# Performance work log

Hardware: AMD Instinct MI355X
Metric: run time of the kernel (lower is better)

The kernel has to match this reference:

```python
import math
import jax, jax.numpy as jnp
import numpy as np

# ---- static configuration (mirrors init_kwargs / chosen shapes) ----
MUL = 16          # multiplicity in "16x0e+16x1e+16x2e"
B_CFG = 64        # number of configurations in batch
N_ATOM = 64       # atoms per configuration
N_NODES = B_CFG * N_ATOM
N_PAIRS = B_CFG * N_ATOM * N_ATOM

# ---- real Wigner 3j symbols (e3nn convention), computed once in numpy ----
def _su2_cg(j1, m1, j2, m2, j3, m3):
    if m3 != m1 + m2:
        return 0.0
    f = math.factorial
    vmin = max(-j1 + j2 + m3, -j1 + m1, 0)
    vmax = min(j2 + j3 + m1, j3 - j1 + j2, j3 + m3)
    C = math.sqrt((2 * j3 + 1) * f(j3 + j1 - j2) * f(j3 - j1 + j2) * f(j1 + j2 - j3)
                  * f(j3 + m3) * f(j3 - m3)
                  / (f(j1 + j2 + j3 + 1) * f(j1 - m1) * f(j1 + m1) * f(j2 - m2) * f(j2 + m2)))
    S = 0.0
    for v in range(vmin, vmax + 1):
        S += (-1) ** (v + j2 + m2) * f(j2 + j3 + m1 - v) * f(j1 - m1 + v) / (
            f(v) * f(j3 - j1 + j2 - v) * f(j3 + m3 - v) * f(v + j1 - j2 - m3))
    return C * S

def _q_real_to_complex(l):
    q = np.zeros((2 * l + 1, 2 * l + 1), dtype=np.complex128)
    for m in range(-l, 0):
        q[l + m, l + abs(m)] = 1 / 2 ** 0.5
        q[l + m, l - abs(m)] = -1j / 2 ** 0.5
    q[l, l] = 1.0
    for m in range(1, l + 1):
        q[l + m, l + abs(m)] = (-1) ** m / 2 ** 0.5
        q[l + m, l - abs(m)] = 1j * (-1) ** m / 2 ** 0.5
    return (-1j) ** l * q

def _wigner_3j(l1, l2, l3):
    C = np.zeros((2 * l1 + 1, 2 * l2 + 1, 2 * l3 + 1))
    for m1 in range(-l1, l1 + 1):
        for m2 in range(-l2, l2 + 1):
            m3 = m1 + m2
            if abs(m3) <= l3:
                C[l1 + m1, l2 + m2, l3 + m3] = _su2_cg(l1, m1, l2, m2, l3, m3)
    Q1, Q2, Q3 = _q_real_to_complex(l1), _q_real_to_complex(l2), _q_real_to_complex(l3)
    Cr = np.einsum('ij,kl,mn,ikm->jln', Q1, Q2, np.conj(Q3), C.astype(np.complex128))
    assert np.abs(Cr.imag).max() < 1e-6
    Cr = Cr.real
    return Cr / np.linalg.norm(Cr)

# all CG paths (l1, l2, l_out) of the fully connected TP (0e+1e+2e)^2 -> 0e+1e+2e
PATHS = [(0, 0, 0), (1, 1, 0), (2, 2, 0),
         (0, 1, 1), (1, 0, 1), (1, 1, 1), (1, 2, 1), (2, 1, 1), (2, 2, 1),
         (0, 2, 2), (2, 0, 2), (1, 1, 2), (1, 2, 2), (2, 1, 2), (2, 2, 2)]
W3J = {p: _wigner_3j(*p) for p in set(PATHS)}
FAN = {lo: sum(1 for p in PATHS if p[2] == lo) * MUL * MUL for lo in (0, 1, 2)}
ALPHA = {lo: math.sqrt(2 * lo + 1) / math.sqrt(FAN[lo]) for lo in (0, 1, 2)}
# CartesianTensor('ij=ij') change of basis: x_ij = sum_{l,m} QCART[lm,i,j] * irreps[lm]
QCART = np.concatenate([math.sqrt(2 * l + 1) * np.transpose(_wigner_3j(1, 1, l), (2, 0, 1))
                        for l in (0, 1, 2)], axis=0)  # (9, 3, 3), orthonormal rows


def setup_inputs() -> dict:
    key = jax.random.key(0)
    k1, k2 = jax.random.split(key)
    node_feats = jax.random.normal(k1, (N_NODES, MUL * 9), dtype=jnp.float32)
    # layout: for each config, all (i, j) atom pairs with global node indices
    ii, jj = jnp.meshgrid(jnp.arange(N_ATOM, dtype=jnp.int32),
                          jnp.arange(N_ATOM, dtype=jnp.int32), indexing='ij')
    base = (jnp.arange(B_CFG, dtype=jnp.int32) * N_ATOM)[:, None, None]
    rows = (base + ii[None]).reshape(-1)
    cols = (base + jj[None]).reshape(-1)
    layout = jnp.stack([rows, cols], axis=1)  # (N_PAIRS, 2) int32
    tp_weights = jax.random.normal(k2, (len(PATHS), MUL, MUL), dtype=jnp.float32)
    return {'node_feats': node_feats, 'layout': layout, 'tp_weights': tp_weights}


def _split(x):
    # (E, MUL*9) -> {l: (E, MUL, 2l+1)} in irreps order 16x0e | 16x1e | 16x2e
    E = x.shape[0]
    return {0: x[:, :MUL].reshape(E, MUL, 1),
            1: x[:, MUL:4 * MUL].reshape(E, MUL, 3),
            2: x[:, 4 * MUL:].reshape(E, MUL, 5)}


def _forward(node_feats, tp_weights, layout):
    x1 = _split(node_feats[layout[:, 0]])   # gather row atoms
    x2 = _split(node_feats[layout[:, 1]])   # gather column atoms
    E = layout.shape[0]
    dt = node_feats.dtype
    out = {lo: jnp.zeros((E, 2 * lo + 1), dt) for lo in (0, 1, 2)}
    for p, (l1, l2, lo) in enumerate(PATHS):
        w3j = jnp.asarray(W3J[(l1, l2, lo)], dt)
        t = jnp.einsum('eui,uv->evi', x1[l1], tp_weights[p])          # mix multiplicities
        out[lo] = out[lo] + ALPHA[lo] * jnp.einsum('evi,evj,ijk->ek', t, x2[l2], w3j)
    irr = jnp.concatenate([out[0], out[1], out[2]], axis=1)           # (E, 9) = 0e+1e+2e
    cart = jnp.einsum('ek,kij->eij', irr, jnp.asarray(QCART, dt))     # (E, 3, 3)
    # symmetrize: (H + H^T)/2 on the 3n x 3n per-config Hessian
    c = cart.reshape(B_CFG, N_ATOM, N_ATOM, 3, 3)
    c = 0.5 * (c + jnp.transpose(c, (0, 2, 1, 4, 3)))
    return c.reshape(E, 3, 3)


def reference(node_feats, layout, tp_weights):
    return _forward(node_feats, tp_weights, layout)
```

## Files before the change

### kernel.cpp

```cpp
#include <hip/hip_runtime.h>
#include <math.h>


#define NPATH 15

constexpr double cfact(int n){ double r = 1.0; for (int i = 2; i <= n; ++i) r *= (double)i; return r; }
constexpr double csqrt(double x){
  if (x <= 0.0) return 0.0;
  double g = x < 1.0 ? 1.0 : x;
  for (int i = 0; i < 64; ++i) g = 0.5*(g + x/g);
  return g;
}

constexpr double ccg(int j1,int m1,int j2,int m2,int j3,int m3){
  if (m3 != m1 + m2) return 0.0;
  int vmin = -j1 + j2 + m3;
  if (-j1 + m1 > vmin) vmin = -j1 + m1;
  if (0 > vmin) vmin = 0;
  int vmax = j2 + j3 + m1;
  if (j3 - j1 + j2 < vmax) vmax = j3 - j1 + j2;
  if (j3 + m3 < vmax) vmax = j3 + m3;
  double C = csqrt((2.0*j3+1.0)*cfact(j3+j1-j2)*cfact(j3-j1+j2)*cfact(j1+j2-j3)
                   *cfact(j3+m3)*cfact(j3-m3)
                   /(cfact(j1+j2+j3+1)*cfact(j1-m1)*cfact(j1+m1)*cfact(j2-m2)*cfact(j2+m2)));
  double S = 0.0;
  for (int v = vmin; v <= vmax; ++v){
    double term = cfact(j2+j3+m1-v)*cfact(j1-m1+v)
                /(cfact(v)*cfact(j3-j1+j2-v)*cfact(j3+m3-v)*cfact(v+j1-j2-m3));
    S += ((v + j2 + m2) & 1) ? -term : term;
  }
  return C * S;
}

struct QM { double re[5][5]; double im[5][5]; };
constexpr QM cbuild_q(int l){
  QM q{};
  double s = 1.0 / csqrt(2.0);
  for (int m = -l; m < 0; ++m){
    q.re[l+m][l-m] = s;
    q.im[l+m][l+m] = -s;
  }
  q.re[l][l] = 1.0;
  for (int m = 1; m <= l; ++m){
    double sg = (m & 1) ? -1.0 : 1.0;
    q.re[l+m][l+m] = sg * s;
    q.im[l+m][l-m] = sg * s;
  }
  if (l == 1){
    for (int r = 0; r < 5; ++r)
      for (int c = 0; c < 5; ++c){
        double a = q.re[r][c], b = q.im[r][c];
        q.re[r][c] = b; q.im[r][c] = -a;
      }
  } else if (l == 2){
    for (int r = 0; r < 5; ++r)
      for (int c = 0; c < 5; ++c){ q.re[r][c] = -q.re[r][c]; q.im[r][c] = -q.im[r][c]; }
  }
  return q;
}

struct CRP { double v[125]; };
constexpr CRP make_cr(int l1, int l2, int l3){
  QM q1 = cbuild_q(l1), q2 = cbuild_q(l2), q3 = cbuild_q(l3);
  const int d1 = 2*l1+1, d2 = 2*l2+1, d3 = 2*l3+1;
  double CG[125] = {};
  for (int i = 0; i < d1; ++i)
    for (int k = 0; k < d2; ++k)
      for (int m = 0; m < d3; ++m)
        CG[(i*5 + k)*5 + m] = ccg(l1, i-l1, l2, k-l2, l3, m-l3);
  CRP o{};
  for (int j = 0; j < d1; ++j)
    for (int l = 0; l < d2; ++l)
      for (int n = 0; n < d3; ++n){
        double acc = 0.0;
        for (int i = 0; i < d1; ++i)
          for (int k = 0; k < d2; ++k)
            for (int m = 0; m < d3; ++m){
              double c = CG[(i*5 + k)*5 + m];
              if (c == 0.0) continue;
              double are = q1.re[i][j], aim = q1.im[i][j];
              double bre = q2.re[k][l], bim = q2.im[k][l];
              double tre = are*bre - aim*bim;
              double tim = are*bim + aim*bre;
              double cre = q3.re[m][n], cim = q3.im[m][n];
              acc += (tre*cre + tim*cim) * c;
            }
        o.v[(j*d2 + l)*d3 + n] = acc;
      }
  double s2 = 0.0;
  for (int e = 0; e < d1*d2*d3; ++e) s2 += o.v[e]*o.v[e];
  double inv = 1.0 / csqrt(s2);
  for (int e = 0; e < d1*d2*d3; ++e) o.v[e] *= inv;
  return o;
}

constexpr CRP CR0  = make_cr(0,0,0);
constexpr CRP CR1  = make_cr(1,1,0);
constexpr CRP CR2  = make_cr(2,2,0);
constexpr CRP CR3  = make_cr(0,1,1);
constexpr CRP CR4  = make_cr(1,0,1);
constexpr CRP CR5  = make_cr(1,1,1);
constexpr CRP CR6  = make_cr(1,2,1);
constexpr CRP CR7  = make_cr(2,1,1);
constexpr CRP CR8  = make_cr(2,2,1);
constexpr CRP CR9  = make_cr(0,2,2);
constexpr CRP CR10 = make_cr(2,0,2);
constexpr CRP CR11 = make_cr(1,1,2);
constexpr CRP CR12 = make_cr(1,2,2);
constexpr CRP CR13 = make_cr(2,1,2);
constexpr CRP CR14 = make_cr(2,2,2);

struct QCT { double v[81]; };
constexpr QCT make_qc(){
  QCT q{};
  for (int lm = 0; lm < 9; ++lm){
    int l = (lm == 0) ? 0 : ((lm < 4) ? 1 : 2);
    int m = lm - l*l;
    const CRP& cr = (l == 0) ? CR1 : ((l == 1) ? CR5 : CR11);
    double sc = csqrt(2.0*l + 1.0);
    for (int r = 0; r < 9; ++r)
      q.v[lm*9 + r] = cr.v[r*(2*l+1) + m] * sc;
  }
  return q;
}
constexpr QCT QCt = make_qc();

struct WQT { float b8[189*8]; float b1[189]; };
constexpr WQT make_wq(){
  WQT t{};
  const CRP* crs[NPATH] = {&CR0,&CR1,&CR2,&CR3,&CR4,&CR5,&CR6,&CR7,&CR8,&CR9,
                           &CR10,&CR11,&CR12,&CR13,&CR14};
  const int L1[NPATH]   = {0,1,2,0,1,1,1,2,2,0,2,1,1,2,2};
  const int L2[NPATH]   = {0,1,2,1,0,1,2,1,2,2,0,1,2,1,2};
  const int LO[NPATH]   = {0,0,0,1,1,1,1,1,1,2,2,2,2,2,2};
  const int PROW[NPATH] = {0,1,10,35,38,41,50,65,80,105,110,115,124,139,164};
  const double AL[3] = { csqrt(1.0/768.0), csqrt(3.0/1536.0), csqrt(5.0/1536.0) };
  for (int p = 0; p < NPATH; ++p){
    const int d1 = 2*L1[p]+1, d2 = 2*L2[p]+1, d3 = 2*LO[p]+1, lo = LO[p];
    for (int i = 0; i < d1; ++i)
      for (int j = 0; j < d2; ++j)
        for (int a = 0; a < 9; ++a){
          double acc = 0.0;
          for (int m = 0; m < d3; ++m)
            acc += crs[p]->v[(i*d2 + j)*d3 + m] * QCt.v[(lo*lo + m)*9 + a];
          double val = AL[lo] * acc;
          int row = PROW[p] + i*d2 + j;
          if (a < 8) t.b8[row*8 + a] = (float)val;
          else       t.b1[row]       = (float)val;
        }
  }
  return t;
}
__constant__ WQT cWQ = make_wq();

__constant__ int cP_L1[NPATH]   = {0,1,2,0,1,1,1,2,2,0,2,1,1,2,2};
__constant__ int cC2P[51] = {0, 1,1,1, 2,2,2,2,2, 3, 4,4,4, 5,5,5, 6,6,6,
                             7,7,7,7,7, 8,8,8,8,8, 9, 10,10,10,10,10,
                             11,11,11, 12,12,12, 13,13,13,13,13, 14,14,14,14,14};
__constant__ int cC2I[51] = {0, 0,1,2, 0,1,2,3,4, 0, 0,1,2, 0,1,2, 0,1,2,
                             0,1,2,3,4, 0,1,2,3,4, 0, 0,1,2,3,4,
                             0,1,2, 0,1,2, 0,1,2,3,4, 0,1,2,3,4};

#define MQ_STRIDE 1296

#define ACCP(TOFF_, PROW_, D1_)                                              \
  { _Pragma("unroll")                                                        \
    for (int i = 0; i < (D1_); ++i){                                         \
      float tv = pT[((TOFF_) + i) * 16 + v];                                 \
      int row = (PROW_) + i * D2 + j;                                        \
      const float4 m0 = *(const float4*)&sB8[row * 8];                       \
      const float4 m1 = *(const float4*)&sB8[row * 8 + 4];                   \
      const float  m8 = sB1[row];                                            \
      acc[0] += tv*m0.x; acc[1] += tv*m0.y; acc[2] += tv*m0.z;               \
      acc[3] += tv*m0.w; acc[4] += tv*m1.x; acc[5] += tv*m1.y;               \
      acc[6] += tv*m1.z; acc[7] += tv*m1.w; acc[8] += tv*m8;                 \
    } }

__global__ __launch_bounds__(256, 4) void mq_kernel(
    const float* __restrict__ feats,
    const int*   __restrict__ layout,
    const float* __restrict__ tpw,
    float*       __restrict__ mqg)
{
  __shared__ __align__(16) float sB8[189 * 8];
  __shared__ float sB1[192];
  __shared__ __align__(16) float sT[4][816];
  __shared__ __align__(16) float sMq[4][1296];
  const int tid  = threadIdx.x;
  const int wave = tid >> 6;
  const int lane = tid & 63;

  for (int o = tid; o < 1512; o += 256) sB8[o] = cWQ.b8[o];
  if (tid < 189) sB1[tid] = cWQ.b1[tid];

  const int rw = blockIdx.x * 4 + wave;
  int rowNode = layout[2 * (rw * 64)];
  rowNode = __builtin_amdgcn_readfirstlane(rowNode);
  const float* __restrict__ x1 = feats + (size_t)rowNode * 144;

  float* __restrict__ pT = sT[wave];
  {
    const int v  = lane & 15;
    const int cq = lane >> 4;
    for (int it = 0; it < 13; ++it){
      int c = cq + it * 4;
      if (c < 51){
        int p = cC2P[c], i = cC2I[c];
        int l1 = cP_L1[p];
        int st = 2*l1 + 1;
        int loff = (l1 == 0) ? 0 : ((l1 == 1) ? 16 : 64);
        const float* xb = x1 + loff + i;
        const float* wb = tpw + p * 256 + v;
        float s = 0.f;
        #pragma unroll
        for (int u = 0; u < 16; ++u) s += xb[u * st] * wb[u * 16];
        pT[c * 16 + v] = s;
      }
    }
  }

  __syncthreads();

  float* __restrict__ pM = sMq[wave];
  for (int rnd = 0; rnd < 3; ++rnd){
    int c = lane + rnd * 64;
    if (c >= 144) break;
    float acc[9];
    #pragma unroll
    for (int a = 0; a < 9; ++a) acc[a] = 0.f;
    if (c < 16){
      const int v = c, j = 0;
      const int D2 = 1;
      ACCP(0,  0,   1)
      ACCP(10, 38,  3)
      ACCP(30, 110, 5)
    } else if (c < 64){
      const int v = (c - 16) / 3, j = (c - 16) % 3;
      const int D2 = 3;
      ACCP(1,  1,   3)
      ACCP(9,  35,  1)
      ACCP(13, 41,  3)
      ACCP(19, 65,  5)
      ACCP(35, 115, 3)
      ACCP(41, 139, 5)
    } else {
      const int v = (c - 64) / 5, j = (c - 64) % 5;
      const int D2 = 5;
      ACCP(4,  10,  5)
      ACCP(16, 50,  3)
      ACCP(24, 80,  5)
      ACCP(29, 105, 1)
      ACCP(38, 124, 3)
      ACCP(46, 164, 5)
    }
    #pragma unroll
    for (int a = 0; a < 9; ++a) pM[c * 9 + a] = acc[a];
  }

  float* __restrict__ dst = mqg + (size_t)rw * MQ_STRIDE;
  #pragma unroll
  for (int r = 0; r < 6; ++r){
    int idx = lane + r * 64;
    if (idx < 324){
      float4 vv = *(const float4*)(pM + idx * 4);
      *(float4*)(dst + idx * 4) = vv;
    }
  }
}

__global__ __launch_bounds__(256) void cart_kernel(
    const float* __restrict__ feats,
    const int*   __restrict__ layout,
    const float* __restrict__ mqg,
    float*       __restrict__ out)
{
  __shared__ float sX2T[144 * 65];
  __shared__ int   sCol[64];
  __shared__ __align__(16) float sOut[4][576];
  const int tid  = threadIdx.x;
  const int wave = tid >> 6;
  const int lane = tid & 63;
  const int rwBase = blockIdx.x * 4;

  if (tid < 64) sCol[tid] = layout[2 * ((size_t)rwBase * 64 + tid) + 1];
  __syncthreads();

  #pragma unroll
  for (int k = 0; k < 9; ++k){
    int q = k * 256 + tid;
    int j = q / 36, c4 = q - j * 36;
    const float4 xv = *(const float4*)(feats + (size_t)sCol[j] * 144 + c4 * 4);
    int c0 = c4 * 4;
    sX2T[(c0+0)*65 + j] = xv.x;
    sX2T[(c0+1)*65 + j] = xv.y;
    sX2T[(c0+2)*65 + j] = xv.z;
    sX2T[(c0+3)*65 + j] = xv.w;
  }
  __syncthreads();

  const int rw = __builtin_amdgcn_readfirstlane(rwBase + wave);
  const float* __restrict__ mq = mqg + (size_t)rw * MQ_STRIDE;

  float acc[9];
  #pragma unroll
  for (int a = 0; a < 9; ++a) acc[a] = 0.f;

  #pragma unroll 8
  for (int c = 0; c < 144; ++c){
    float x = sX2T[c * 65 + lane];
    #pragma unroll
    for (int a = 0; a < 9; ++a) acc[a] += x * mq[c * 9 + a];
  }

  float* __restrict__ pO = sOut[wave];
  #pragma unroll
  for (int a = 0; a < 9; ++a) pO[lane * 9 + a] = acc[a];
  float* __restrict__ ob = out + (size_t)rw * 576;
  #pragma unroll
  for (int r = 0; r < 3; ++r){
    int idx = lane + r * 64;
    if (idx < 144){
      float4 vv = *(const float4*)(pO + idx * 4);
      *(float4*)(ob + idx * 4) = vv;
    }
  }
}

__global__ __launch_bounds__(256, 4) void fused_kernel(
    const float* __restrict__ feats,
    const int*   __restrict__ layout,
    const float* __restrict__ tpw,
    float*       __restrict__ out)
{
  __shared__ __align__(16) float sB8[189 * 8];
  __shared__ float sB1[192];
  __shared__ __align__(16) float sT[4][816];
  __shared__ __align__(16) float sMqT[4][1296];
  const int tid  = threadIdx.x;
  const int wave = tid >> 6;
  const int lane = tid & 63;

  for (int o = tid; o < 1512; o += 256) sB8[o] = cWQ.b8[o];
  if (tid < 189) sB1[tid] = cWQ.b1[tid];

  const int rw = blockIdx.x * 4 + wave;
  const int e0 = rw * 64;
  int rowNode = layout[2 * e0];
  rowNode = __builtin_amdgcn_readfirstlane(rowNode);
  const float* __restrict__ x1 = feats + (size_t)rowNode * 144;

  float* __restrict__ pT = sT[wave];
  {
    const int v  = lane & 15;
    const int cq = lane >> 4;
    for (int it = 0; it < 13; ++it){
      int c = cq + it * 4;
      if (c < 51){
        int p = cC2P[c], i = cC2I[c];
        int l1 = cP_L1[p];
        int st = 2*l1 + 1;
        int loff = (l1 == 0) ? 0 : ((l1 == 1) ? 16 : 64);
        const float* xb = x1 + loff + i;
        const float* wb = tpw + p * 256 + v;
        float s = 0.f;
        #pragma unroll
        for (int u = 0; u < 16; ++u) s += xb[u * st] * wb[u * 16];
        pT[c * 16 + v] = s;
      }
    }
  }
  __syncthreads();

  float* __restrict__ pM = sMqT[wave];
  for (int rnd = 0; rnd < 3; ++rnd){
    int c = lane + rnd * 64;
    if (c >= 144) break;
    float acc[9];
    #pragma unroll
    for (int a = 0; a < 9; ++a) acc[a] = 0.f;
    if (c < 16){
      const int v = c, j = 0;
      const int D2 = 1;
      ACCP(0,  0,   1)
      ACCP(10, 38,  3)
      ACCP(30, 110, 5)
    } else if (c < 64){
      const int v = (c - 16) / 3, j = (c - 16) % 3;
      const int D2 = 3;
      ACCP(1,  1,   3)
      ACCP(9,  35,  1)
      ACCP(13, 41,  3)
      ACCP(19, 65,  5)
      ACCP(35, 115, 3)
      ACCP(41, 139, 5)
    } else {
      const int v = (c - 64) / 5, j = (c - 64) % 5;
      const int D2 = 5;
      ACCP(4,  10,  5)
      ACCP(16, 50,  3)
      ACCP(24, 80,  5)
      ACCP(29, 105, 1)
      ACCP(38, 124, 3)
      ACCP(46, 164, 5)
    }
    #pragma unroll
    for (int a = 0; a < 9; ++a) pM[a * 144 + c] = acc[a];
  }

  const size_t e = (size_t)e0 + lane;
  const int col = layout[2 * e + 1];
  const float* __restrict__ x2 = feats + (size_t)col * 144;

  float acc[9];
  #pragma unroll
  for (int a = 0; a < 9; ++a) acc[a] = 0.f;

  for (int cc = 0; cc < 36; ++cc){
    const float4 x = *(const float4*)(x2 + cc * 4);
    const float* mb = pM + cc * 4;
    #pragma unroll
    for (int a = 0; a < 9; ++a){
      float4 mv = *(const float4*)(mb + a * 144);
      acc[a] += x.x*mv.x + x.y*mv.y + x.z*mv.z + x.w*mv.w;
    }
  }

  #pragma unroll
  for (int a = 0; a < 9; ++a) pT[lane * 9 + a] = acc[a];
  float* ob = out + (size_t)e0 * 9;
  #pragma unroll
  for (int r = 0; r < 3; ++r){
    int idx = lane + r * 64;
    if (idx < 144){
      float4 vv = *(const float4*)(pT + idx * 4);
      *(float4*)(ob + idx * 4) = vv;
    }
  }
}

__global__ __launch_bounds__(256) void sym_tiled(float* __restrict__ out){
  __shared__ float sA[16 * 145];
  __shared__ float sB[16 * 145];
  const int tid = threadIdx.x;
  const int b  = blockIdx.x / 10;
  const int tp = blockIdx.x - b * 10;
  const int TI[10] = {0,0,0,0,1,1,1,2,2,3};
  const int TJ[10] = {0,1,2,3,1,2,3,2,3,3};
  const int ti = TI[tp], tj = TJ[tp];
  const bool diag = (ti == tj);
  const size_t cfgBase = (size_t)b * 4096 * 9;

  for (int idx = tid; idx < 2304; idx += 256){
    int r = idx / 144, off = idx - r * 144;
    sA[r * 145 + off] = out[cfgBase + ((size_t)(ti*16 + r) * 64 + tj*16) * 9 + off];
  }
  if (!diag){
    for (int idx = tid; idx < 2304; idx += 256){
      int r = idx / 144, off = idx - r * 144;
      sB[r * 145 + off] = out[cfgBase + ((size_t)(tj*16 + r) * 64 + ti*16) * 9 + off];
    }
  }
  __syncthreads();

  const int di = tid >> 4, dj = tid & 15;
  const float* A = sA;
  const float* B = diag ? sA : sB;
  float oa[9], ob[9];
  #pragma unroll
  for (int a = 0; a < 3; ++a)
    #pragma unroll
    for (int d = 0; d < 3; ++d){
      oa[a*3+d] = 0.5f * (A[di*145 + dj*9 + a*3+d] + B[dj*145 + di*9 + d*3+a]);
      if (!diag)
        ob[a*3+d] = 0.5f * (B[di*145 + dj*9 + a*3+d] + A[dj*145 + di*9 + d*3+a]);
    }
  __syncthreads();

  #pragma unroll
  for (int r9 = 0; r9 < 9; ++r9) sA[di*145 + dj*9 + r9] = oa[r9];
  if (!diag){
    #pragma unroll
    for (int r9 = 0; r9 < 9; ++r9) sB[di*145 + dj*9 + r9] = ob[r9];
  }
  __syncthreads();

  for (int idx = tid; idx < 2304; idx += 256){
    int r = idx / 144, off = idx - r * 144;
    out[cfgBase + ((size_t)(ti*16 + r) * 64 + tj*16) * 9 + off] = sA[r * 145 + off];
  }
  if (!diag){
    for (int idx = tid; idx < 2304; idx += 256){
      int r = idx / 144, off = idx - r * 144;
      out[cfgBase + ((size_t)(tj*16 + r) * 64 + ti*16) * 9 + off] = sB[r * 145 + off];
    }
  }
}

extern "C" void kernel_launch(void* const* d_in, const int* in_sizes, int n_in,
                              void* d_out, int out_size, void* d_ws, size_t ws_size,
                              hipStream_t stream) {
  const float* feats  = (const float*)d_in[0];
  const int*   layout = (const int*)  d_in[1];
  const float* tpw    = (const float*)d_in[2];
  float* out = (float*)d_out;
  float* ws  = (float*)d_ws;

  const int E = in_sizes[1] / 2;
  const int R = E / 64;
  const int B = E / 4096;

  const size_t need = (size_t)R * MQ_STRIDE * sizeof(float);
  if (ws_size >= need){
    float* mqg = ws;
    mq_kernel  <<<R / 4, 256, 0, stream>>>(feats, layout, tpw, mqg);
    cart_kernel<<<R / 4, 256, 0, stream>>>(feats, layout, mqg, out);
  } else {
    fused_kernel<<<R / 4, 256, 0, stream>>>(feats, layout, tpw, out);
  }
  sym_tiled<<<B * 10, 256, 0, stream>>>(out);
}
```

Measured before the change: 124.0 us.

## Fuse mq and cart kernels into one shared-memory kernel, dropping workspace round trip

```diff
diff --git a/kernel.cpp b/kernel.cpp
--- a/kernel.cpp
+++ b/kernel.cpp
@@ -161,8 +161,6 @@
                              0,1,2,3,4, 0,1,2,3,4, 0, 0,1,2,3,4,
                              0,1,2, 0,1,2, 0,1,2,3,4, 0,1,2,3,4};
 
-#define MQ_STRIDE 1296
-
 #define ACCP(TOFF_, PROW_, D1_)                                              \
   { _Pragma("unroll")                                                        \
     for (int i = 0; i < (D1_); ++i){                                         \
@@ -176,41 +174,53 @@
       acc[6] += tv*m1.z; acc[7] += tv*m1.w; acc[8] += tv*m8;                 \
     } }
 
-__global__ __launch_bounds__(256, 4) void mq_kernel(
+__global__ __launch_bounds__(256, 2) void fused2_kernel(
     const float* __restrict__ feats,
     const int*   __restrict__ layout,
     const float* __restrict__ tpw,
-    float*       __restrict__ mqg)
+    float*       __restrict__ out)
 {
-  __shared__ __align__(16) float sB8[189 * 8];
-  __shared__ float sB1[192];
-  __shared__ __align__(16) float sT[4][816];
-  __shared__ __align__(16) float sMq[4][1296];
+  __shared__ __align__(16) float U[11664];
+  __shared__ __align__(16) float sMq[4][1728];
+  __shared__ __align__(16) float sX1[4][144];
+  __shared__ int sCol[64];
+
   const int tid  = threadIdx.x;
   const int wave = tid >> 6;
   const int lane = tid & 63;
+  const int rwBase = blockIdx.x * 4;
+
+  float* sB8  = U;
+  float* sB1  = U + 1512;
+  float* sTPW = U + 4968;
 
   for (int o = tid; o < 1512; o += 256) sB8[o] = cWQ.b8[o];
   if (tid < 189) sB1[tid] = cWQ.b1[tid];
-
-  const int rw = blockIdx.x * 4 + wave;
-  int rowNode = layout[2 * (rw * 64)];
-  rowNode = __builtin_amdgcn_readfirstlane(rowNode);
-  const float* __restrict__ x1 = feats + (size_t)rowNode * 144;
-
-  float* __restrict__ pT = sT[wave];
+  for (int q = tid; q < 960; q += 256)
+    *(float4*)&sTPW[q * 4] = ((const float4*)tpw)[q];
+  if (tid < 144){
+    int w = tid / 36, q = tid - w * 36;
+    int rn = layout[2 * ((rwBase + w) * 64)];
+    *(float4*)&sX1[w][q * 4] = *(const float4*)(feats + (size_t)rn * 144 + q * 4);
+  }
+  if (tid >= 192)
+    sCol[tid - 192] = layout[2 * ((size_t)rwBase * 64 + (tid - 192)) + 1];
+  __syncthreads();
+
+  float* pT = U + 1704 + wave * 816;
   {
     const int v  = lane & 15;
     const int cq = lane >> 4;
+    const float* xw = sX1[wave];
     for (int it = 0; it < 13; ++it){
       int c = cq + it * 4;
       if (c < 51){
         int p = cC2P[c], i = cC2I[c];
         int l1 = cP_L1[p];
-        int st = 2*l1 + 1;
+        int st = 2 * l1 + 1;
         int loff = (l1 == 0) ? 0 : ((l1 == 1) ? 16 : 64);
-        const float* xb = x1 + loff + i;
-        const float* wb = tpw + p * 256 + v;
+        const float* xb = xw + loff + i;
+        const float* wb = sTPW + p * 256 + v;
         float s = 0.f;
         #pragma unroll
         for (int u = 0; u < 16; ++u) s += xb[u * st] * wb[u * 16];
@@ -219,9 +229,7 @@
     }
   }
 
-  __syncthreads();
-
-  float* __restrict__ pM = sMq[wave];
+  float* pM = sMq[wave];
   for (int rnd = 0; rnd < 3; ++rnd){
     int c = lane + rnd * 64;
     if (c >= 144) break;
@@ -253,53 +261,25 @@
       ACCP(38, 124, 3)
       ACCP(46, 164, 5)
     }
-    #pragma unroll
-    for (int a = 0; a < 9; ++a) pM[c * 9 + a] = acc[a];
-  }
-
-  float* __restrict__ dst = mqg + (size_t)rw * MQ_STRIDE;
-  #pragma unroll
-  for (int r = 0; r < 6; ++r){
-    int idx = lane + r * 64;
-    if (idx < 324){
-      float4 vv = *(const float4*)(pM + idx * 4);
-      *(float4*)(dst + idx * 4) = vv;
-    }
-  }
-}
-
-__global__ __launch_bounds__(256) void cart_kernel(
-    const float* __restrict__ feats,
-    const int*   __restrict__ layout,
-    const float* __restrict__ mqg,
-    float*       __restrict__ out)
-{
-  __shared__ float sX2T[144 * 65];
-  __shared__ int   sCol[64];
-  __shared__ __align__(16) float sOut[4][576];
-  const int tid  = threadIdx.x;
-  const int wave = tid >> 6;
-  const int lane = tid & 63;
-  const int rwBase = blockIdx.x * 4;
-
-  if (tid < 64) sCol[tid] = layout[2 * ((size_t)rwBase * 64 + tid) + 1];
-  __syncthreads();
-
+    *(float4*)&pM[c * 12]     = make_float4(acc[0], acc[1], acc[2], acc[3]);
+    *(float4*)&pM[c * 12 + 4] = make_float4(acc[4], acc[5], acc[6], acc[7]);
+    pM[c * 12 + 8] = acc[8];
+  }
+  __syncthreads();
+
+  float* sX2T = U;
   #pragma unroll
   for (int k = 0; k < 9; ++k){
     int q = k * 256 + tid;
     int j = q / 36, c4 = q - j * 36;
     const float4 xv = *(const float4*)(feats + (size_t)sCol[j] * 144 + c4 * 4);
     int c0 = c4 * 4;
-    sX2T[(c0+0)*65 + j] = xv.x;
-    sX2T[(c0+1)*65 + j] = xv.y;
-    sX2T[(c0+2)*65 + j] = xv.z;
-    sX2T[(c0+3)*65 + j] = xv.w;
-  }
-  __syncthreads();
-
-  const int rw = __builtin_amdgcn_readfirstlane(rwBase + wave);
-  const float* __restrict__ mq = mqg + (size_t)rw * MQ_STRIDE;
+    sX2T[(c0 + 0) * 65 + j] = xv.x;
+    sX2T[(c0 + 1) * 65 + j] = xv.y;
+    sX2T[(c0 + 2) * 65 + j] = xv.z;
+    sX2T[(c0 + 3) * 65 + j] = xv.w;
+  }
+  __syncthreads();
 
   float acc[9];
   #pragma unroll
@@ -308,131 +288,23 @@
   #pragma unroll 8
   for (int c = 0; c < 144; ++c){
     float x = sX2T[c * 65 + lane];
-    #pragma unroll
-    for (int a = 0; a < 9; ++a) acc[a] += x * mq[c * 9 + a];
-  }
-
-  float* __restrict__ pO = sOut[wave];
+    const float4 m0 = *(const float4*)&pM[c * 12];
+    const float4 m1 = *(const float4*)&pM[c * 12 + 4];
+    const float  m8 = pM[c * 12 + 8];
+    acc[0] += x * m0.x; acc[1] += x * m0.y; acc[2] += x * m0.z;
+    acc[3] += x * m0.w; acc[4] += x * m1.x; acc[5] += x * m1.y;
+    acc[6] += x * m1.z; acc[7] += x * m1.w; acc[8] += x * m8;
+  }
+
+  float* pO = U + 9360 + wave * 576;
   #pragma unroll
   for (int a = 0; a < 9; ++a) pO[lane * 9 + a] = acc[a];
-  float* __restrict__ ob = out + (size_t)rw * 576;
+  float* ob = out + (size_t)(rwBase + wave) * 576;
   #pragma unroll
   for (int r = 0; r < 3; ++r){
     int idx = lane + r * 64;
     if (idx < 144){
       float4 vv = *(const float4*)(pO + idx * 4);
-      *(float4*)(ob + idx * 4) = vv;
-    }
-  }
-}
-
-__global__ __launch_bounds__(256, 4) void fused_kernel(
-    const float* __restrict__ feats,
-    const int*   __restrict__ layout,
-    const float* __restrict__ tpw,
-    float*       __restrict__ out)
-{
-  __shared__ __align__(16) float sB8[189 * 8];
-  __shared__ float sB1[192];
-  __shared__ __align__(16) float sT[4][816];
-  __shared__ __align__(16) float sMqT[4][1296];
-  const int tid  = threadIdx.x;
-  const int wave = tid >> 6;
-  const int lane = tid & 63;
-
-  for (int o = tid; o < 1512; o += 256) sB8[o] = cWQ.b8[o];
-  if (tid < 189) sB1[tid] = cWQ.b1[tid];
-
-  const int rw = blockIdx.x * 4 + wave;
-  const int e0 = rw * 64;
-  int rowNode = layout[2 * e0];
-  rowNode = __builtin_amdgcn_readfirstlane(rowNode);
-  const float* __restrict__ x1 = feats + (size_t)rowNode * 144;
-
-  float* __restrict__ pT = sT[wave];
-  {
-    const int v  = lane & 15;
-    const int cq = lane >> 4;
-    for (int it = 0; it < 13; ++it){
-      int c = cq + it * 4;
-      if (c < 51){
-        int p = cC2P[c], i = cC2I[c];
-        int l1 = cP_L1[p];
-        int st = 2*l1 + 1;
-        int loff = (l1 == 0) ? 0 : ((l1 == 1) ? 16 : 64);
-        const float* xb = x1 + loff + i;
-        const float* wb = tpw + p * 256 + v;
-        float s = 0.f;
-        #pragma unroll
-        for (int u = 0; u < 16; ++u) s += xb[u * st] * wb[u * 16];
-        pT[c * 16 + v] = s;
-      }
-    }
-  }
-  __syncthreads();
-
-  float* __restrict__ pM = sMqT[wave];
-  for (int rnd = 0; rnd < 3; ++rnd){
-    int c = lane + rnd * 64;
-    if (c >= 144) break;
-    float acc[9];
-    #pragma unroll
-    for (int a = 0; a < 9; ++a) acc[a] = 0.f;
-    if (c < 16){
-      const int v = c, j = 0;
-      const int D2 = 1;
-      ACCP(0,  0,   1)
-      ACCP(10, 38,  3)
-      ACCP(30, 110, 5)
-    } else if (c < 64){
-      const int v = (c - 16) / 3, j = (c - 16) % 3;
-      const int D2 = 3;
-      ACCP(1,  1,   3)
-      ACCP(9,  35,  1)
-      ACCP(13, 41,  3)
-      ACCP(19, 65,  5)
-      ACCP(35, 115, 3)
-      ACCP(41, 139, 5)
-    } else {
-      const int v = (c - 64) / 5, j = (c - 64) % 5;
-      const int D2 = 5;
-      ACCP(4,  10,  5)
-      ACCP(16, 50,  3)
-      ACCP(24, 80,  5)
-      ACCP(29, 105, 1)
-      ACCP(38, 124, 3)
-      ACCP(46, 164, 5)
-    }
-    #pragma unroll
-    for (int a = 0; a < 9; ++a) pM[a * 144 + c] = acc[a];
-  }
-
-  const size_t e = (size_t)e0 + lane;
-  const int col = layout[2 * e + 1];
-  const float* __restrict__ x2 = feats + (size_t)col * 144;
-
-  float acc[9];
-  #pragma unroll
-  for (int a = 0; a < 9; ++a) acc[a] = 0.f;
-
-  for (int cc = 0; cc < 36; ++cc){
-    const float4 x = *(const float4*)(x2 + cc * 4);
-    const float* mb = pM + cc * 4;
-    #pragma unroll
-    for (int a = 0; a < 9; ++a){
-      float4 mv = *(const float4*)(mb + a * 144);
-      acc[a] += x.x*mv.x + x.y*mv.y + x.z*mv.z + x.w*mv.w;
-    }
-  }
-
-  #pragma unroll
-  for (int a = 0; a < 9; ++a) pT[lane * 9 + a] = acc[a];
-  float* ob = out + (size_t)e0 * 9;
-  #pragma unroll
-  for (int r = 0; r < 3; ++r){
-    int idx = lane + r * 64;
-    if (idx < 144){
-      float4 vv = *(const float4*)(pT + idx * 4);
       *(float4*)(ob + idx * 4) = vv;
     }
   }
@@ -503,19 +375,12 @@
   const int*   layout = (const int*)  d_in[1];
   const float* tpw    = (const float*)d_in[2];
   float* out = (float*)d_out;
-  float* ws  = (float*)d_ws;
+  (void)d_ws; (void)ws_size; (void)n_in; (void)out_size;
 
   const int E = in_sizes[1] / 2;
   const int R = E / 64;
   const int B = E / 4096;
 
-  const size_t need = (size_t)R * MQ_STRIDE * sizeof(float);
-  if (ws_size >= need){
-    float* mqg = ws;
-    mq_kernel  <<<R / 4, 256, 0, stream>>>(feats, layout, tpw, mqg);
-    cart_kernel<<<R / 4, 256, 0, stream>>>(feats, layout, mqg, out);
-  } else {
-    fused_kernel<<<R / 4, 256, 0, stream>>>(feats, layout, tpw, out);
-  }
+  fused2_kernel<<<R / 4, 256, 0, stream>>>(feats, layout, tpw, out);
   sym_tiled<<<B * 10, 256, 0, stream>>>(out);
 }
```

After: 112.5 us. -9.3%, faster.
